# Kernel tuning notes

Measured on AMD Instinct MI355X. Metric: run time of the kernel, lower is better.

The kernel has to match this reference:

```python
import jax, jax.numpy as jnp
import numpy as np

B, L, D = 2, 2048, 1024
H, HD = 16, 64          # heads, head size; inner = H*HD = 1024
FF = 4 * D              # 4096; GeGLU first linear outputs 2*FF
EPS_SCALE = 0.1         # LayerScale eps for depth=12 (<=18)


def layer_norm(x, g, b, eps=1e-5):
    mu = jnp.mean(x, axis=-1, keepdims=True)
    var = jnp.var(x, axis=-1, keepdims=True)
    return (x - mu) * jax.lax.rsqrt(var + eps) * g + b


def setup_inputs() -> dict:
    key = jax.random.key(0)
    ks = jax.random.split(key, 8)
    std_qkv = np.sqrt(2.0 / (D + HD)).astype(np.float32)
    return {
        "x": jax.random.normal(ks[0], (B, L, D), jnp.float32),
        "mask": jnp.ones((B, L), dtype=bool),
        "w_qkv": jax.random.normal(ks[1], (D, 3 * H * HD), jnp.float32) * std_qkv,
        "w_out": jax.random.normal(ks[2], (H * HD, D), jnp.float32) * np.sqrt(2.0 / (H * HD + D)).astype(np.float32),
        "b_out": jnp.zeros((D,), jnp.float32),
        "ln_inner_g": jnp.ones((D,), jnp.float32),
        "ln_inner_b": jnp.zeros((D,), jnp.float32),
        "ln_pre_attn_g": jnp.ones((D,), jnp.float32),
        "ln_pre_attn_b": jnp.zeros((D,), jnp.float32),
        "scale_attn": jnp.full((1, 1, D), EPS_SCALE, jnp.float32),
        "w1": jax.random.normal(ks[3], (D, 2 * FF), jnp.float32) * (1.0 / np.sqrt(D).astype(np.float32)),
        "b1": jnp.zeros((2 * FF,), jnp.float32),
        "w2": jax.random.normal(ks[4], (FF, D), jnp.float32) * (1.0 / np.sqrt(FF).astype(np.float32)),
        "b2": jnp.zeros((D,), jnp.float32),
        "ln_pre_ff_g": jnp.ones((D,), jnp.float32),
        "ln_pre_ff_b": jnp.zeros((D,), jnp.float32),
        "scale_ff": jnp.full((1, 1, D), EPS_SCALE, jnp.float32),
    }


def reference(x, mask, w_qkv, w_out, b_out, ln_inner_g, ln_inner_b,
              ln_pre_attn_g, ln_pre_attn_b, scale_attn,
              w1, b1, w2, b2, ln_pre_ff_g, ln_pre_ff_b, scale_ff):
    # ---- attention block: LayerScale(PreNorm(MHA)) -- NO residual add ----
    h = layer_norm(x, ln_pre_attn_g, ln_pre_attn_b)
    qkv = h @ w_qkv                                   # [B,L,3*H*HD]
    q, k, v = jnp.split(qkv, 3, axis=-1)
    def to_heads(t):
        return t.reshape(B, L, H, HD).transpose(0, 2, 1, 3)  # [B,H,L,HD]
    q, k, v = to_heads(q), to_heads(k), to_heads(v)
    dots = jnp.einsum('bhid,bhjd->bhij', q, k) / np.sqrt(HD).astype(np.float32)
    dots = jnp.where(mask[:, None, None, :], dots, -jnp.inf)
    attn = jax.nn.softmax(dots, axis=-1)
    out = jnp.einsum('bhij,bhjd->bhid', attn, v)      # [B,H,L,HD]
    out = out.transpose(0, 2, 1, 3).reshape(B, L, H * HD)
    out = out @ w_out + b_out
    out = layer_norm(out, ln_inner_g, ln_inner_b)     # extra LN inside MHA
    x = out * scale_attn
    # ---- FFN block: LayerScale(PreNorm(GeGLU FFN)) -- NO residual add ----
    h = layer_norm(x, ln_pre_ff_g, ln_pre_ff_b)
    u = h @ w1 + b1                                   # [B,L,2*FF]
    a, g = jnp.split(u, 2, axis=-1)
    ff = (a * jax.nn.gelu(g, approximate=False)) @ w2 + b2
    x = ff * scale_ff
    return x
```

## Files before the change

### kernel.cpp

```cpp
#include <hip/hip_runtime.h>
#include <hip/hip_bf16.h>
#include <math.h>

typedef __bf16 bf16;
typedef float  floatx4 __attribute__((ext_vector_type(4)));
typedef bf16   bf16x8  __attribute__((ext_vector_type(8)));
typedef bf16   bf16x4  __attribute__((ext_vector_type(4)));

#define L_TOK 2048
#define D_MOD 1024

__device__ __forceinline__ floatx4 mfma16x16x32(bf16x8 a, bf16x8 b, floatx4 c) {
    return __builtin_amdgcn_mfma_f32_16x16x32_bf16(a, b, c, 0, 0, 0);
}

__device__ __forceinline__ void async_load16(const bf16* gptr, const bf16* lptr) {
    __builtin_amdgcn_global_load_lds(
        (const __attribute__((address_space(1))) unsigned int*)gptr,
        (__attribute__((address_space(3))) unsigned int*)lptr,
        16, 0, 0);
}

__device__ __forceinline__ int swz_col(int e) {
    const int r = e >> 5;
    return (((e >> 3) & 3) ^ ((r >> 1) & 3)) << 3;
}

__device__ __forceinline__ void block_red2(float& s, float& s2, float* red, int tid) {
    #pragma unroll
    for (int off = 32; off > 0; off >>= 1) {
        s  += __shfl_down(s,  off, 64);
        s2 += __shfl_down(s2, off, 64);
    }
    __syncthreads();
    if ((tid & 63) == 0) { red[tid >> 6] = s; red[4 + (tid >> 6)] = s2; }
    __syncthreads();
    s  = red[0] + red[1] + red[2] + red[3];
    s2 = red[4] + red[5] + red[6] + red[7];
}

__global__ __launch_bounds__(256) void transpose_all(
    const float* __restrict__ w_qkv, const float* __restrict__ w_out,
    const float* __restrict__ w1,    const float* __restrict__ w2,
    bf16* __restrict__ wqkvT, bf16* __restrict__ woutT,
    bf16* __restrict__ w1T,   bf16* __restrict__ w2T)
{
    __shared__ float t[32][33];
    int id = blockIdx.x;
    const float* src; bf16* dst; int R, C, bx, by;
    if (id < 3072)       { src = w_qkv; dst = wqkvT; R = 1024; C = 3072; bx = id % 96;  by = id / 96;  }
    else if (id < 4096)  { id -= 3072;  src = w_out; dst = woutT; R = 1024; C = 1024; bx = id % 32;  by = id / 32;  }
    else if (id < 12288) { id -= 4096;  src = w1;    dst = w1T;   R = 1024; C = 8192; bx = id % 256; by = id / 256; }
    else                 { id -= 12288; src = w2;    dst = w2T;   R = 4096; C = 1024; bx = id % 32;  by = id / 32;  }
    const int tx = threadIdx.x & 31, ty = threadIdx.x >> 5;
    const int c0 = bx * 32, r0 = by * 32;
    #pragma unroll
    for (int i = 0; i < 4; ++i)
        t[ty + i * 8][tx] = src[(size_t)(r0 + ty + i * 8) * C + c0 + tx];
    __syncthreads();
    #pragma unroll
    for (int i = 0; i < 4; ++i)
        dst[(size_t)(c0 + ty + i * 8) * R + r0 + tx] = (bf16)t[tx][ty + i * 8];
}

__global__ __launch_bounds__(256) void transpose_v(
    const bf16* __restrict__ qkv, bf16* __restrict__ vt)
{
    __shared__ bf16 t[32][33];
    const int tx = threadIdx.x & 31, ty = threadIdx.x >> 5;
    const int bh = blockIdx.z, b = bh >> 4, h = bh & 15;
    const int l0 = blockIdx.x * 32, hd0 = blockIdx.y * 32;
    const bf16* src = qkv + (size_t)b * L_TOK * 3072 + 2048 + h * 64;
    bf16* dst = vt + (size_t)bh * 64 * 2048;
    #pragma unroll
    for (int i = 0; i < 4; ++i)
        t[ty + i * 8][tx] = src[(size_t)(l0 + ty + i * 8) * 3072 + hd0 + tx];
    __syncthreads();
    #pragma unroll
    for (int i = 0; i < 4; ++i)
        dst[(size_t)(hd0 + ty + i * 8) * 2048 + l0 + tx] = t[tx][ty + i * 8];
}

__global__ __launch_bounds__(256) void ln_rows(
    const float* __restrict__ x, const float* __restrict__ gw,
    const float* __restrict__ bw, bf16* __restrict__ outp)
{
    const int row = blockIdx.x, tid = threadIdx.x;
    const int c0 = tid * 4;
    __shared__ float red[8];
    const float4 xv = *(const float4*)(x + (size_t)row * D_MOD + c0);
    float v[4] = {xv.x, xv.y, xv.z, xv.w};
    float s = 0.f, s2 = 0.f;
    #pragma unroll
    for (int i = 0; i < 4; ++i) { s += v[i]; s2 += v[i] * v[i]; }
    block_red2(s, s2, red, tid);
    const float mu = s * (1.f / D_MOD);
    const float rs = rsqrtf(s2 * (1.f / D_MOD) - mu * mu + 1e-5f);
    bf16x4 ov;
    #pragma unroll
    for (int i = 0; i < 4; ++i) {
        const int c = c0 + i;
        ov[i] = (bf16)((v[i] - mu) * rs * gw[c] + bw[c]);
    }
    *(bf16x4*)(outp + (size_t)row * D_MOD + c0) = ov;
}

__global__ __launch_bounds__(256) void ln_fuse(
    const float* __restrict__ in,
    const float* __restrict__ g1, const float* __restrict__ b1v,
    const float* __restrict__ sc,
    const float* __restrict__ g2, const float* __restrict__ b2v,
    bf16* __restrict__ outp)
{
    const int row = blockIdx.x, tid = threadIdx.x;
    const int c0 = tid * 4;
    __shared__ float red[8];
    const float4 xv = *(const float4*)(in + (size_t)row * D_MOD + c0);
    float v[4] = {xv.x, xv.y, xv.z, xv.w};
    float s = 0.f, s2 = 0.f;
    #pragma unroll
    for (int i = 0; i < 4; ++i) { s += v[i]; s2 += v[i] * v[i]; }
    block_red2(s, s2, red, tid);
    const float mu = s * (1.f / D_MOD);
    const float rs = rsqrtf(s2 * (1.f / D_MOD) - mu * mu + 1e-5f);
    float x2[4], t = 0.f, t2 = 0.f;
    #pragma unroll
    for (int i = 0; i < 4; ++i) {
        const int c = c0 + i;
        const float y = (v[i] - mu) * rs * g1[c] + b1v[c];
        x2[i] = y * sc[c];
        t += x2[i]; t2 += x2[i] * x2[i];
    }
    block_red2(t, t2, red, tid);
    const float mu2 = t * (1.f / D_MOD);
    const float rs2 = rsqrtf(t2 * (1.f / D_MOD) - mu2 * mu2 + 1e-5f);
    bf16x4 ov;
    #pragma unroll
    for (int i = 0; i < 4; ++i) {
        const int c = c0 + i;
        ov[i] = (bf16)((x2[i] - mu2) * rs2 * g2[c] + b2v[c]);
    }
    *(bf16x4*)(outp + (size_t)row * D_MOD + c0) = ov;
}

__global__ __launch_bounds__(256) void gemm_bt(
    const bf16* __restrict__ A, const bf16* __restrict__ Bt,
    void* __restrict__ Cout,
    const float* __restrict__ bias, const float* __restrict__ aux,
    int M, int N, int K, int mode)
{
    __shared__ __align__(16) bf16 lA[4096];
    __shared__ __align__(16) bf16 lB[4096];
    const int tid  = threadIdx.x;
    const int wave = tid >> 6, lane = tid & 63;
    const int lrow = lane & 15, quad = lane >> 4;
    const int wm = wave >> 1, wn = wave & 1;
    const int rowBase = blockIdx.y * 128;
    const int colBase = blockIdx.x * 128;

    floatx4 acc[4][4];
    const floatx4 vzero = {0.f, 0.f, 0.f, 0.f};
    #pragma unroll
    for (int i = 0; i < 4; ++i)
        #pragma unroll
        for (int j = 0; j < 4; ++j) acc[i][j] = vzero;

    const int e0 = wave * 1024 + lane * 8;
    const int r0 = e0 >> 5, c0 = swz_col(e0);
    const int e1 = e0 + 512;
    const int r1 = e1 >> 5, c1 = swz_col(e1);
    bf16* dstA0 = lA + wave * 1024;
    bf16* dstA1 = lA + wave * 1024 + 512;
    bf16* dstB0 = lB + wave * 1024;
    bf16* dstB1 = lB + wave * 1024 + 512;

    const int sx = (quad ^ ((lrow >> 1) & 3)) << 3;
    const bf16* paBase = lA + (wm * 64 + lrow) * 32 + sx;
    const bf16* pbBase = lB + (wn * 64 + lrow) * 32 + sx;

    const int nk = K >> 5;
    for (int kb = 0; kb < nk; ++kb) {
        const int k0 = kb << 5;
        __syncthreads();
        async_load16(A  + (size_t)(rowBase + r0) * K + k0 + c0, dstA0);
        async_load16(A  + (size_t)(rowBase + r1) * K + k0 + c1, dstA1);
        async_load16(Bt + (size_t)(colBase + r0) * K + k0 + c0, dstB0);
        async_load16(Bt + (size_t)(colBase + r1) * K + k0 + c1, dstB1);
        __syncthreads();
        bf16x8 af[4], bfv[4];
        #pragma unroll
        for (int i = 0; i < 4; ++i) af[i]  = *(const bf16x8*)(paBase + i * 512);
        #pragma unroll
        for (int i = 0; i < 4; ++i) bfv[i] = *(const bf16x8*)(pbBase + i * 512);
        #pragma unroll
        for (int mi = 0; mi < 4; ++mi)
            #pragma unroll
            for (int ni = 0; ni < 4; ++ni)
                acc[mi][ni] = mfma16x16x32(af[mi], bfv[ni], acc[mi][ni]);
    }

    #pragma unroll
    for (int mi = 0; mi < 4; ++mi) {
        #pragma unroll
        for (int ni = 0; ni < 4; ++ni) {
            const int col = colBase + wn * 64 + ni * 16 + lrow;
            const float bv = bias ? bias[col] : 0.f;
            #pragma unroll
            for (int r = 0; r < 4; ++r) {
                const int row = rowBase + wm * 64 + mi * 16 + quad * 4 + r;
                const size_t idx = (size_t)row * N + col;
                const float v = acc[mi][ni][r];
                if (mode == 0) ((bf16*)Cout)[idx] = (bf16)v;
                else           ((float*)Cout)[idx] = v + bv;
            }
        }
    }
    (void)aux;
}

__global__ __launch_bounds__(256) void gemm_bt64(
    const bf16* __restrict__ A, const bf16* __restrict__ Bt,
    float* __restrict__ Cout,
    const float* __restrict__ bias, const float* __restrict__ aux,
    int M, int N, int K, int mode)
{
    __shared__ __align__(16) bf16 lA[2048];
    __shared__ __align__(16) bf16 lB[4096];
    const int tid  = threadIdx.x;
    const int wave = tid >> 6, lane = tid & 63;
    const int lrow = lane & 15, quad = lane >> 4;
    const int wm = wave >> 1, wn = wave & 1;
    const int rowBase = blockIdx.y * 64;
    const int colBase = blockIdx.x * 128;

    floatx4 acc[2][4];
    const floatx4 vzero = {0.f, 0.f, 0.f, 0.f};
    #pragma unroll
    for (int i = 0; i < 2; ++i)
        #pragma unroll
        for (int j = 0; j < 4; ++j) acc[i][j] = vzero;

    const int eA = wave * 512 + lane * 8;
    const int rA = eA >> 5, cA = swz_col(eA);
    const int e0 = wave * 1024 + lane * 8;
    const int r0 = e0 >> 5, c0 = swz_col(e0);
    const int e1 = e0 + 512;
    const int r1 = e1 >> 5, c1 = swz_col(e1);

    const int sx = (quad ^ ((lrow >> 1) & 3)) << 3;
    const bf16* paBase = lA + (wm * 32 + lrow) * 32 + sx;
    const bf16* pbBase = lB + (wn * 64 + lrow) * 32 + sx;

    const int nk = K >> 5;
    for (int kb = 0; kb < nk; ++kb) {
        const int k0 = kb << 5;
        __syncthreads();
        async_load16(A  + (size_t)(rowBase + rA) * K + k0 + cA, lA + wave * 512);
        async_load16(Bt + (size_t)(colBase + r0) * K + k0 + c0, lB + wave * 1024);
        async_load16(Bt + (size_t)(colBase + r1) * K + k0 + c1, lB + wave * 1024 + 512);
        __syncthreads();
        bf16x8 af[2], bfv[4];
        #pragma unroll
        for (int i = 0; i < 2; ++i) af[i]  = *(const bf16x8*)(paBase + i * 512);
        #pragma unroll
        for (int i = 0; i < 4; ++i) bfv[i] = *(const bf16x8*)(pbBase + i * 512);
        #pragma unroll
        for (int mi = 0; mi < 2; ++mi)
            #pragma unroll
            for (int ni = 0; ni < 4; ++ni)
                acc[mi][ni] = mfma16x16x32(af[mi], bfv[ni], acc[mi][ni]);
    }

    #pragma unroll
    for (int mi = 0; mi < 2; ++mi) {
        #pragma unroll
        for (int ni = 0; ni < 4; ++ni) {
            const int col = colBase + wn * 64 + ni * 16 + lrow;
            const float bv = bias[col];
            const float sv = (mode == 4) ? aux[col] : 1.f;
            #pragma unroll
            for (int r = 0; r < 4; ++r) {
                const int row = rowBase + wm * 32 + mi * 16 + quad * 4 + r;
                const float v = acc[mi][ni][r] + bv;
                Cout[(size_t)row * N + col] = (mode == 4) ? v * sv : v;
            }
        }
    }
}

__global__ __launch_bounds__(256, 2) void gemm_geglu(
    const bf16* __restrict__ A, const bf16* __restrict__ Bta,
    const bf16* __restrict__ Btg, bf16* __restrict__ Cout,
    const float* __restrict__ ba, const float* __restrict__ bg,
    int M, int N, int K)
{
    __shared__ __align__(16) bf16 lA[4096];
    __shared__ __align__(16) bf16 lBa[4096];
    __shared__ __align__(16) bf16 lBg[4096];
    const int tid  = threadIdx.x;
    const int wave = tid >> 6, lane = tid & 63;
    const int lrow = lane & 15, quad = lane >> 4;
    const int wm = wave >> 1, wn = wave & 1;
    const int rowBase = blockIdx.y * 128;
    const int colBase = blockIdx.x * 128;

    floatx4 aa[4][4], ag[4][4];
    const floatx4 vzero = {0.f, 0.f, 0.f, 0.f};
    #pragma unroll
    for (int i = 0; i < 4; ++i)
        #pragma unroll
        for (int j = 0; j < 4; ++j) { aa[i][j] = vzero; ag[i][j] = vzero; }

    const int e0 = wave * 1024 + lane * 8;
    const int r0 = e0 >> 5, c0 = swz_col(e0);
    const int e1 = e0 + 512;
    const int r1 = e1 >> 5, c1 = swz_col(e1);
    const int sx = (quad ^ ((lrow >> 1) & 3)) << 3;
    const int fragOff  = (wm * 64 + lrow) * 32 + sx;
    const int fragOffB = (wn * 64 + lrow) * 32 + sx;

    const int nk = K >> 5;
    for (int kb = 0; kb < nk; ++kb) {
        const int k0 = kb << 5;
        __syncthreads();
        async_load16(A   + (size_t)(rowBase + r0) * K + k0 + c0, lA  + wave * 1024);
        async_load16(A   + (size_t)(rowBase + r1) * K + k0 + c1, lA  + wave * 1024 + 512);
        async_load16(Bta + (size_t)(colBase + r0) * K + k0 + c0, lBa + wave * 1024);
        async_load16(Bta + (size_t)(colBase + r1) * K + k0 + c1, lBa + wave * 1024 + 512);
        async_load16(Btg + (size_t)(colBase + r0) * K + k0 + c0, lBg + wave * 1024);
        async_load16(Btg + (size_t)(colBase + r1) * K + k0 + c1, lBg + wave * 1024 + 512);
        __syncthreads();
        bf16x8 af[4], bA[4], bG[4];
        #pragma unroll
        for (int i = 0; i < 4; ++i) af[i] = *(const bf16x8*)(lA  + fragOff  + i * 512);
        #pragma unroll
        for (int i = 0; i < 4; ++i) bA[i] = *(const bf16x8*)(lBa + fragOffB + i * 512);
        #pragma unroll
        for (int i = 0; i < 4; ++i) bG[i] = *(const bf16x8*)(lBg + fragOffB + i * 512);
        #pragma unroll
        for (int mi = 0; mi < 4; ++mi)
            #pragma unroll
            for (int ni = 0; ni < 4; ++ni) {
                aa[mi][ni] = mfma16x16x32(af[mi], bA[ni], aa[mi][ni]);
                ag[mi][ni] = mfma16x16x32(af[mi], bG[ni], ag[mi][ni]);
            }
    }

    #pragma unroll
    for (int mi = 0; mi < 4; ++mi) {
        #pragma unroll
        for (int ni = 0; ni < 4; ++ni) {
            const int col = colBase + wn * 64 + ni * 16 + lrow;
            const float bva = ba[col], bvg = bg[col];
            #pragma unroll
            for (int r = 0; r < 4; ++r) {
                const int row = rowBase + wm * 64 + mi * 16 + quad * 4 + r;
                const float av = aa[mi][ni][r] + bva;
                const float gv = ag[mi][ni][r] + bvg;
                const float gel = 0.5f * gv * (1.f + erff(gv * 0.70710678f));
                Cout[(size_t)row * N + col] = (bf16)(av * gel);
            }
        }
    }
}

__global__ __launch_bounds__(256, 2) void attn_fwd(
    const bf16* __restrict__ qkv, const bf16* __restrict__ vt,
    bf16* __restrict__ outp)
{
    const int tid  = threadIdx.x;
    const int wave = tid >> 6, lane = tid & 63;
    const int lrow = lane & 15, quad = lane >> 4;
    const int bh = blockIdx.x >> 4, qg = blockIdx.x & 15;
    const int b = bh >> 4, h = bh & 15;

    __shared__ float oM[64][129];
    __shared__ float lM[128];

    bf16x8 qf[8][2];
    {
        const bf16* qbase = qkv + ((size_t)(b * L_TOK + qg * 128 + lrow)) * 3072
                          + h * 64 + quad * 8;
        #pragma unroll
        for (int qt = 0; qt < 8; ++qt) {
            const bf16* qp = qbase + (size_t)qt * 16 * 3072;
            qf[qt][0] = *(const bf16x8*)qp;
            qf[qt][1] = *(const bf16x8*)(qp + 32);
        }
    }

    const int koff = ((lrow >> 2) << 3) + (lrow & 3);
    const bf16* kbase = qkv + (size_t)b * L_TOK * 3072 + 1024 + h * 64 + quad * 8;
    const bf16* vbase = vt + ((size_t)bh * 64 + lrow) * 2048 + quad * 8;

    float l_part[8];
    #pragma unroll
    for (int i = 0; i < 8; ++i) l_part[i] = 0.f;
    const floatx4 vzero = {0.f, 0.f, 0.f, 0.f};
    floatx4 o[8][4];
    #pragma unroll
    for (int qt = 0; qt < 8; ++qt)
        #pragma unroll
        for (int ni = 0; ni < 4; ++ni) o[qt][ni] = vzero;

    const int k0w = wave * 512;
    for (int kb = k0w; kb < k0w + 512; kb += 32) {
        const bf16* kp0 = kbase + (size_t)(kb + koff) * 3072;
        const bf16* kp1 = kbase + (size_t)(kb + koff + 4) * 3072;
        const bf16x8 ka0 = *(const bf16x8*)kp0;
        const bf16x8 kb0 = *(const bf16x8*)(kp0 + 32);
        const bf16x8 ka1 = *(const bf16x8*)kp1;
        const bf16x8 kb1 = *(const bf16x8*)(kp1 + 32);
        const bf16* vp = vbase + kb;
        bf16x8 va[4];
        #pragma unroll
        for (int ni = 0; ni < 4; ++ni)
            va[ni] = *(const bf16x8*)(vp + (size_t)ni * 16 * 2048);

        #pragma unroll
        for (int qt = 0; qt < 8; ++qt) {
            floatx4 st0 = vzero, st1 = vzero;
            st0 = mfma16x16x32(ka0, qf[qt][0], st0);
            st0 = mfma16x16x32(kb0, qf[qt][1], st0);
            st1 = mfma16x16x32(ka1, qf[qt][0], st1);
            st1 = mfma16x16x32(kb1, qf[qt][1], st1);
            bf16x8 pb;
            #pragma unroll
            for (int r = 0; r < 4; ++r) {
                const float p = __expf(fmaf(st0[r], 0.125f, -8.0f));
                l_part[qt] += p;
                pb[r] = (bf16)p;
            }
            #pragma unroll
            for (int r = 0; r < 4; ++r) {
                const float p = __expf(fmaf(st1[r], 0.125f, -8.0f));
                l_part[qt] += p;
                pb[4 + r] = (bf16)p;
            }
            #pragma unroll
            for (int ni = 0; ni < 4; ++ni)
                o[qt][ni] = mfma16x16x32(va[ni], pb, o[qt][ni]);
        }
    }

    #pragma unroll
    for (int qt = 0; qt < 8; ++qt) {
        l_part[qt] += __shfl_xor(l_part[qt], 16, 64);
        l_part[qt] += __shfl_xor(l_part[qt], 32, 64);
    }

    for (int w = 0; w < 4; ++w) {
        if (wave == w) {
            #pragma unroll
            for (int qt = 0; qt < 8; ++qt) {
                const int q = qt * 16 + lrow;
                #pragma unroll
                for (int ni = 0; ni < 4; ++ni) {
                    #pragma unroll
                    for (int r = 0; r < 4; ++r) {
                        const int d = ni * 16 + quad * 4 + r;
                        if (w == 0) oM[d][q] = o[qt][ni][r];
                        else        oM[d][q] += o[qt][ni][r];
                    }
                }
                if (quad == 0) {
                    if (w == 0) lM[q] = l_part[qt];
                    else        lM[q] += l_part[qt];
                }
            }
        }
        __syncthreads();
    }

    for (int it = tid; it < 2048; it += 256) {
        const int q = it >> 4, dg = it & 15;
        const float inv = 1.f / lM[q];
        bf16x4 ov;
        #pragma unroll
        for (int r = 0; r < 4; ++r) ov[r] = (bf16)(oM[dg * 4 + r][q] * inv);
        const size_t row = (size_t)b * L_TOK + qg * 128 + q;
        *(bf16x4*)(outp + row * 1024 + h * 64 + dg * 4) = ov;
    }
}

extern "C" void kernel_launch(void* const* d_in, const int* in_sizes, int n_in,
                              void* d_out, int out_size, void* d_ws, size_t ws_size,
                              hipStream_t stream) {
    const float* x       = (const float*)d_in[0];
    const float* w_qkv   = (const float*)d_in[2];
    const float* w_out   = (const float*)d_in[3];
    const float* b_out   = (const float*)d_in[4];
    const float* ln_in_g = (const float*)d_in[5];
    const float* ln_in_b = (const float*)d_in[6];
    const float* ln_pa_g = (const float*)d_in[7];
    const float* ln_pa_b = (const float*)d_in[8];
    const float* sc_attn = (const float*)d_in[9];
    const float* w1      = (const float*)d_in[10];
    const float* b1      = (const float*)d_in[11];
    const float* w2      = (const float*)d_in[12];
    const float* b2      = (const float*)d_in[13];
    const float* ln_ff_g = (const float*)d_in[14];
    const float* ln_ff_b = (const float*)d_in[15];
    const float* sc_ff   = (const float*)d_in[16];
    float* outp = (float*)d_out;
    (void)in_sizes; (void)n_in; (void)out_size; (void)ws_size;

    char* ws = (char*)d_ws;
    const size_t MB = 1024 * 1024;
    bf16*  w1T      = (bf16*) (ws + 0 * MB);
    bf16*  w2T      = (bf16*) (ws + 16 * MB);
    bf16*  hbuf     = (bf16*) (ws + 24 * MB);
    bf16*  vtb      = (bf16*) (ws + 32 * MB);
    bf16*  qkvb     = (bf16*) (ws + 40 * MB);
    bf16*  wqkvT    = (bf16*) (ws + 64 * MB);
    bf16*  attn_o   = (bf16*) (ws + 64 * MB);
    float* out_proj = (float*)(ws + 72 * MB);
    bf16*  woutT    = (bf16*) (ws + 88 * MB);
    bf16*  ff_in    = (bf16*) (ws + 40 * MB);

    transpose_all<<<16384, 256, 0, stream>>>(w_qkv, w_out, w1, w2,
                                             wqkvT, woutT, w1T, w2T);
    ln_rows<<<4096, 256, 0, stream>>>(x, ln_pa_g, ln_pa_b, hbuf);
    gemm_bt<<<dim3(24, 32), 256, 0, stream>>>(hbuf, wqkvT, qkvb, nullptr, nullptr,
                                              4096, 3072, 1024, 0);
    transpose_v<<<dim3(64, 2, 32), 256, 0, stream>>>(qkvb, vtb);
    attn_fwd<<<512, 256, 0, stream>>>(qkvb, vtb, attn_o);
    gemm_bt64<<<dim3(8, 64), 256, 0, stream>>>(attn_o, woutT, out_proj, b_out, nullptr,
                                               4096, 1024, 1024, 1);
    ln_fuse<<<4096, 256, 0, stream>>>(out_proj, ln_in_g, ln_in_b, sc_attn,
                                      ln_ff_g, ln_ff_b, hbuf);
    gemm_geglu<<<dim3(32, 32), 256, 0, stream>>>(hbuf, w1T, w1T + (size_t)4096 * 1024,
                                                 ff_in, b1, b1 + 4096, 4096, 4096, 1024);
    gemm_bt64<<<dim3(8, 64), 256, 0, stream>>>(ff_in, w2T, outp, b2, sc_ff,
                                               4096, 1024, 4096, 4);
}
```

Baseline: 447.3 us.

## Split-K the final FFN GEMM and narrow GeGLU tiles for higher occupancy

The final down-projection GEMM (K=4096) is split into two K halves via a z grid dimension, writing two fp32 partial buffers that a new combine kernel sums with bias and LayerScale. The GeGLU GEMM tile is narrowed from 128 to 64 columns, halving its B-side shared memory and accumulators and raising the occupancy hint to 3 blocks per CU, with twice as many blocks. Both aim to expose more parallelism and latency hiding on the long-K GEMMs, at the cost of an extra kernel launch, extra partial-sum memory traffic, and less A-tile reuse in GeGLU.

```diff
diff --git a/kernel.cpp b/kernel.cpp
--- a/kernel.cpp
+++ b/kernel.cpp
@@ -146,8 +146,7 @@
 __global__ __launch_bounds__(256) void gemm_bt(
     const bf16* __restrict__ A, const bf16* __restrict__ Bt,
     void* __restrict__ Cout,
-    const float* __restrict__ bias, const float* __restrict__ aux,
-    int M, int N, int K, int mode)
+    int M, int N, int K)
 {
     __shared__ __align__(16) bf16 lA[4096];
     __shared__ __align__(16) bf16 lB[4096];
@@ -204,25 +203,20 @@
         #pragma unroll
         for (int ni = 0; ni < 4; ++ni) {
             const int col = colBase + wn * 64 + ni * 16 + lrow;
-            const float bv = bias ? bias[col] : 0.f;
             #pragma unroll
             for (int r = 0; r < 4; ++r) {
                 const int row = rowBase + wm * 64 + mi * 16 + quad * 4 + r;
-                const size_t idx = (size_t)row * N + col;
-                const float v = acc[mi][ni][r];
-                if (mode == 0) ((bf16*)Cout)[idx] = (bf16)v;
-                else           ((float*)Cout)[idx] = v + bv;
+                ((bf16*)Cout)[(size_t)row * N + col] = (bf16)acc[mi][ni][r];
             }
         }
     }
-    (void)aux;
 }
 
 __global__ __launch_bounds__(256) void gemm_bt64(
     const bf16* __restrict__ A, const bf16* __restrict__ Bt,
-    float* __restrict__ Cout,
-    const float* __restrict__ bias, const float* __restrict__ aux,
-    int M, int N, int K, int mode)
+    float* __restrict__ C0, float* __restrict__ C1,
+    const float* __restrict__ bias,
+    int M, int N, int lda, int Ksub, int mode)
 {
     __shared__ __align__(16) bf16 lA[2048];
     __shared__ __align__(16) bf16 lB[4096];
@@ -232,6 +226,7 @@
     const int wm = wave >> 1, wn = wave & 1;
     const int rowBase = blockIdx.y * 64;
     const int colBase = blockIdx.x * 128;
+    const int kBase   = blockIdx.z * Ksub;
 
     floatx4 acc[2][4];
     const floatx4 vzero = {0.f, 0.f, 0.f, 0.f};
@@ -251,13 +246,13 @@
     const bf16* paBase = lA + (wm * 32 + lrow) * 32 + sx;
     const bf16* pbBase = lB + (wn * 64 + lrow) * 32 + sx;
 
-    const int nk = K >> 5;
+    const int nk = Ksub >> 5;
     for (int kb = 0; kb < nk; ++kb) {
-        const int k0 = kb << 5;
-        __syncthreads();
-        async_load16(A  + (size_t)(rowBase + rA) * K + k0 + cA, lA + wave * 512);
-        async_load16(Bt + (size_t)(colBase + r0) * K + k0 + c0, lB + wave * 1024);
-        async_load16(Bt + (size_t)(colBase + r1) * K + k0 + c1, lB + wave * 1024 + 512);
+        const int k0 = kBase + (kb << 5);
+        __syncthreads();
+        async_load16(A  + (size_t)(rowBase + rA) * lda + k0 + cA, lA + wave * 512);
+        async_load16(Bt + (size_t)(colBase + r0) * lda + k0 + c0, lB + wave * 1024);
+        async_load16(Bt + (size_t)(colBase + r1) * lda + k0 + c1, lB + wave * 1024 + 512);
         __syncthreads();
         bf16x8 af[2], bfv[4];
         #pragma unroll
@@ -271,53 +266,72 @@
                 acc[mi][ni] = mfma16x16x32(af[mi], bfv[ni], acc[mi][ni]);
     }
 
+    float* C = blockIdx.z ? C1 : C0;
     #pragma unroll
     for (int mi = 0; mi < 2; ++mi) {
         #pragma unroll
         for (int ni = 0; ni < 4; ++ni) {
             const int col = colBase + wn * 64 + ni * 16 + lrow;
-            const float bv = bias[col];
-            const float sv = (mode == 4) ? aux[col] : 1.f;
+            const float bv = (mode == 1) ? bias[col] : 0.f;
             #pragma unroll
             for (int r = 0; r < 4; ++r) {
                 const int row = rowBase + wm * 32 + mi * 16 + quad * 4 + r;
-                const float v = acc[mi][ni][r] + bv;
-                Cout[(size_t)row * N + col] = (mode == 4) ? v * sv : v;
+                C[(size_t)row * N + col] = acc[mi][ni][r] + bv;
             }
         }
     }
 }
 
-__global__ __launch_bounds__(256, 2) void gemm_geglu(
+__global__ __launch_bounds__(256) void combine_out(
+    const float* __restrict__ p0, const float* __restrict__ p1,
+    const float* __restrict__ b2, const float* __restrict__ sc,
+    float* __restrict__ outp)
+{
+    const int row = blockIdx.x, c0 = threadIdx.x * 4;
+    const size_t base = (size_t)row * D_MOD + c0;
+    const float4 a = *(const float4*)(p0 + base);
+    const float4 b = *(const float4*)(p1 + base);
+    float4 o;
+    o.x = (a.x + b.x + b2[c0 + 0]) * sc[c0 + 0];
+    o.y = (a.y + b.y + b2[c0 + 1]) * sc[c0 + 1];
+    o.z = (a.z + b.z + b2[c0 + 2]) * sc[c0 + 2];
+    o.w = (a.w + b.w + b2[c0 + 3]) * sc[c0 + 3];
+    *(float4*)(outp + base) = o;
+}
+
+__global__ __launch_bounds__(256, 3) void gemm_geglu(
     const bf16* __restrict__ A, const bf16* __restrict__ Bta,
     const bf16* __restrict__ Btg, bf16* __restrict__ Cout,
     const float* __restrict__ ba, const float* __restrict__ bg,
     int M, int N, int K)
 {
     __shared__ __align__(16) bf16 lA[4096];
-    __shared__ __align__(16) bf16 lBa[4096];
-    __shared__ __align__(16) bf16 lBg[4096];
+    __shared__ __align__(16) bf16 lBa[2048];
+    __shared__ __align__(16) bf16 lBg[2048];
     const int tid  = threadIdx.x;
     const int wave = tid >> 6, lane = tid & 63;
     const int lrow = lane & 15, quad = lane >> 4;
     const int wm = wave >> 1, wn = wave & 1;
     const int rowBase = blockIdx.y * 128;
-    const int colBase = blockIdx.x * 128;
-
-    floatx4 aa[4][4], ag[4][4];
+    const int colBase = blockIdx.x * 64;
+
+    floatx4 aa[4][2], ag[4][2];
     const floatx4 vzero = {0.f, 0.f, 0.f, 0.f};
     #pragma unroll
     for (int i = 0; i < 4; ++i)
         #pragma unroll
-        for (int j = 0; j < 4; ++j) { aa[i][j] = vzero; ag[i][j] = vzero; }
+        for (int j = 0; j < 2; ++j) { aa[i][j] = vzero; ag[i][j] = vzero; }
 
     const int e0 = wave * 1024 + lane * 8;
     const int r0 = e0 >> 5, c0 = swz_col(e0);
     const int e1 = e0 + 512;
     const int r1 = e1 >> 5, c1 = swz_col(e1);
+    const int eB = wave * 512 + lane * 8;
+    const int rB = eB >> 5, cB = swz_col(eB);
+
     const int sx = (quad ^ ((lrow >> 1) & 3)) << 3;
     const int fragOff  = (wm * 64 + lrow) * 32 + sx;
-    const int fragOffB = (wn * 64 + lrow) * 32 + sx;
+    const int fragOffB = (wn * 32 + lrow) * 32 + sx;
 
     const int nk = K >> 5;
     for (int kb = 0; kb < nk; ++kb) {
@@ -325,22 +339,20 @@
         __syncthreads();
         async_load16(A   + (size_t)(rowBase + r0) * K + k0 + c0, lA  + wave * 1024);
         async_load16(A   + (size_t)(rowBase + r1) * K + k0 + c1, lA  + wave * 1024 + 512);
-        async_load16(Bta + (size_t)(colBase + r0) * K + k0 + c0, lBa + wave * 1024);
-        async_load16(Bta + (size_t)(colBase + r1) * K + k0 + c1, lBa + wave * 1024 + 512);
-        async_load16(Btg + (size_t)(colBase + r0) * K + k0 + c0, lBg + wave * 1024);
-        async_load16(Btg + (size_t)(colBase + r1) * K + k0 + c1, lBg + wave * 1024 + 512);
-        __syncthreads();
-        bf16x8 af[4], bA[4], bG[4];
+        async_load16(Bta + (size_t)(colBase + rB) * K + k0 + cB, lBa + wave * 512);
+        async_load16(Btg + (size_t)(colBase + rB) * K + k0 + cB, lBg + wave * 512);
+        __syncthreads();
+        bf16x8 af[4], bA[2], bG[2];
         #pragma unroll
         for (int i = 0; i < 4; ++i) af[i] = *(const bf16x8*)(lA  + fragOff  + i * 512);
         #pragma unroll
-        for (int i = 0; i < 4; ++i) bA[i] = *(const bf16x8*)(lBa + fragOffB + i * 512);
-        #pragma unroll
-        for (int i = 0; i < 4; ++i) bG[i] = *(const bf16x8*)(lBg + fragOffB + i * 512);
+        for (int i = 0; i < 2; ++i) bA[i] = *(const bf16x8*)(lBa + fragOffB + i * 512);
+        #pragma unroll
+        for (int i = 0; i < 2; ++i) bG[i] = *(const bf16x8*)(lBg + fragOffB + i * 512);
         #pragma unroll
         for (int mi = 0; mi < 4; ++mi)
             #pragma unroll
-            for (int ni = 0; ni < 4; ++ni) {
+            for (int ni = 0; ni < 2; ++ni) {
                 aa[mi][ni] = mfma16x16x32(af[mi], bA[ni], aa[mi][ni]);
                 ag[mi][ni] = mfma16x16x32(af[mi], bG[ni], ag[mi][ni]);
             }
@@ -349,8 +361,8 @@
     #pragma unroll
     for (int mi = 0; mi < 4; ++mi) {
         #pragma unroll
-        for (int ni = 0; ni < 4; ++ni) {
-            const int col = colBase + wn * 64 + ni * 16 + lrow;
+        for (int ni = 0; ni < 2; ++ni) {
+            const int col = colBase + wn * 32 + ni * 16 + lrow;
             const float bva = ba[col], bvg = bg[col];
             #pragma unroll
             for (int r = 0; r < 4; ++r) {
@@ -517,20 +529,22 @@
     float* out_proj = (float*)(ws + 72 * MB);
     bf16*  woutT    = (bf16*) (ws + 88 * MB);
     bf16*  ff_in    = (bf16*) (ws + 40 * MB);
+    float* p0       = (float*)(ws + 72 * MB);
+    float* p1       = (float*)(ws + 24 * MB);
 
     transpose_all<<<16384, 256, 0, stream>>>(w_qkv, w_out, w1, w2,
                                              wqkvT, woutT, w1T, w2T);
     ln_rows<<<4096, 256, 0, stream>>>(x, ln_pa_g, ln_pa_b, hbuf);
-    gemm_bt<<<dim3(24, 32), 256, 0, stream>>>(hbuf, wqkvT, qkvb, nullptr, nullptr,
-                                              4096, 3072, 1024, 0);
+    gemm_bt<<<dim3(24, 32), 256, 0, stream>>>(hbuf, wqkvT, qkvb, 4096, 3072, 1024);
     transpose_v<<<dim3(64, 2, 32), 256, 0, stream>>>(qkvb, vtb);
     attn_fwd<<<512, 256, 0, stream>>>(qkvb, vtb, attn_o);
-    gemm_bt64<<<dim3(8, 64), 256, 0, stream>>>(attn_o, woutT, out_proj, b_out, nullptr,
-                                               4096, 1024, 1024, 1);
+    gemm_bt64<<<dim3(8, 64, 1), 256, 0, stream>>>(attn_o, woutT, out_proj, out_proj,
+                                                  b_out, 4096, 1024, 1024, 1024, 1);
     ln_fuse<<<4096, 256, 0, stream>>>(out_proj, ln_in_g, ln_in_b, sc_attn,
                                       ln_ff_g, ln_ff_b, hbuf);
-    gemm_geglu<<<dim3(32, 32), 256, 0, stream>>>(hbuf, w1T, w1T + (size_t)4096 * 1024,
+    gemm_geglu<<<dim3(64, 32), 256, 0, stream>>>(hbuf, w1T, w1T + (size_t)4096 * 1024,
                                                  ff_in, b1, b1 + 4096, 4096, 4096, 1024);
-    gemm_bt64<<<dim3(8, 64), 256, 0, stream>>>(ff_in, w2T, outp, b2, sc_ff,
-                                               4096, 1024, 4096, 4);
-}
+    gemm_bt64<<<dim3(8, 64, 2), 256, 0, stream>>>(ff_in, w2T, p0, p1,
+                                                  nullptr, 4096, 1024, 4096, 2048, 5);
+    combine_out<<<4096, 256, 0, stream>>>(p0, p1, b2, sc_ff, outp);
+}
```

Measured after the change: 434.4 us. 2.9% less time.
